# Optimization experiments

Measured on AMD Instinct MI355X. Metric: run time of the kernel, lower is better.

Reference implementation:

```python
import jax, jax.numpy as jnp
import numpy as np

EPS = 1e-12  # torch F.normalize eps

def _l2norm(v, axis):
    n = jnp.sqrt(jnp.sum(v * v, axis=axis, keepdims=True))
    return v / jnp.maximum(n, EPS)

def setup_inputs() -> dict:
    key = jax.random.key(0)
    k1, k2, k3 = jax.random.split(key, 3)
    B, D, H, W, K = 64, 512, 30, 40, 64
    x = jax.random.normal(k1, (B, D, H, W), dtype=jnp.float32)
    conv_w = jax.random.normal(k2, (K, D), dtype=jnp.float32)  # 1x1 conv weight, no bias (vladv1)
    centroids = jax.random.uniform(k3, (K, D), dtype=jnp.float32)
    return {"x": x, "conv_w": conv_w, "centroids": centroids}

def reference(x, conv_w, centroids):
    B, D, H, W = x.shape
    K = centroids.shape[0]
    # L2-normalize input descriptors over channel dim
    x = _l2norm(x, axis=1)
    xf = x.reshape(B, D, H * W)                       # (B, D, N)
    # 1x1 conv == per-pixel matmul; softmax over clusters
    logits = jnp.einsum('bdn,kd->bkn', xf, conv_w)    # (B, K, N)
    a = jax.nn.softmax(logits, axis=1)                # (B, K, N)
    # VLAD residual aggregation, loop-free:
    # vlad[b,k,d] = sum_n a[b,k,n] * (x[b,d,n] - c[k,d])
    vlad = jnp.einsum('bkn,bdn->bkd', a, xf) - a.sum(axis=-1)[..., None] * centroids[None]
    # intra-normalize per cluster, flatten, global L2 norm
    vlad = _l2norm(vlad, axis=2)
    v = vlad.reshape(B, K * D)
    return _l2norm(v, axis=1)
```

## Files before the change

### kernel.cpp

```cpp
#include <hip/hip_runtime.h>

#define B_ 64
#define D_ 512
#define N_ 1200
#define K_ 64
#define NT2CNT 19
#define AST 1216
#define NT3 16
#define PT 32
#define NTILES 38

typedef unsigned short u16;
typedef __attribute__((ext_vector_type(8))) short bf16x8;
typedef __attribute__((ext_vector_type(8))) unsigned short u16x8;
typedef __attribute__((ext_vector_type(4))) float f32x4;

__device__ __forceinline__ float bf2f(u16 u) {
  union { unsigned int i; float f; } v; v.i = ((unsigned int)u) << 16; return v.f;
}
__device__ __forceinline__ u16 f2bf(float f) {
  unsigned int u = __float_as_uint(f);
  u += 0x7FFFu + ((u >> 16) & 1u);
  return (u16)(u >> 16);
}

__global__ __launch_bounds__(64) void k_wsplit(
    const float* __restrict__ w,
    u16* __restrict__ wfh, u16* __restrict__ wfl)
{
  const int blk = blockIdx.x;
  const int wv = blk >> 4, kk = blk & 15;
  const int l = threadIdx.x;
  const int row = wv * 16 + (l & 15);
  const int dbase = kk * 32 + 8 * (l >> 4);
  const size_t o = ((size_t)blk * 64 + l) * 8;
#pragma unroll
  for (int j = 0; j < 8; ++j) {
    const float v = w[row * D_ + dbase + j];
    const unsigned int u = __float_as_uint(v);
    const unsigned int h = u & 0xFFFF0000u;
    wfh[o + j] = (u16)(h >> 16);
    wfl[o + j] = f2bf(v - __uint_as_float(h));
  }
}

__global__ __launch_bounds__(256, 4) void k_logits_mfma(
    const float* __restrict__ x, const u16* __restrict__ wfh,
    const u16* __restrict__ wfl, u16* __restrict__ a_bf,
    float* __restrict__ invn_ws, float* __restrict__ asum_part, int folded)
{
  const int nt = blockIdx.x, b = blockIdx.y;
  const int n0 = nt * 64;
  const int t = threadIdx.x;
  const int lane = t & 63, wv = t >> 6;

  __shared__ __align__(16) u16 xbuf[2][2][512][8];
  __shared__ float nsq_s[4][64];
  __shared__ float red_s[3][64];
  float (*ls)[66] = reinterpret_cast<float(*)[66]>(&xbuf[0][0][0][0]);

  const int n_l = t & 63, dg = t >> 6;
  const int nc = min(n0 + n_l, N_ - 1);
  const float* xb = x + (size_t)b * D_ * N_ + nc;
  float nsq = 0.f;

  f32x4 acc[4] = {{0.f,0.f,0.f,0.f},{0.f,0.f,0.f,0.f},{0.f,0.f,0.f,0.f},{0.f,0.f,0.f,0.f}};

  const int kkl_w = dg >> 1;
  const int qb    = (dg & 1) * 2;
  const int slotw = kkl_w * 256 + (n_l >> 4) * 64 + qb * 16 + (n_l & 15);

  auto loadf = [&](int c, float* f) {
    const int db = c * 64 + dg * 16;
#pragma unroll
    for (int e = 0; e < 16; ++e) f[e] = xb[(size_t)(db + e) * N_];
  };
  auto cvtwrite = [&](const float* f, int buf) {
    u16x8 h0{}, h1{}, l0{}, l1{};
#pragma unroll
    for (int e = 0; e < 16; ++e) {
      nsq += f[e] * f[e];
      const unsigned int u = __float_as_uint(f[e]);
      const unsigned int hi = u & 0xFFFF0000u;
      const u16 hh = (u16)(hi >> 16);
      const u16 ll = f2bf(f[e] - __uint_as_float(hi));
      if (e < 8) { h0[e] = (short)hh; l0[e] = (short)ll; }
      else       { h1[e - 8] = (short)hh; l1[e - 8] = (short)ll; }
    }
    *(u16x8*)xbuf[buf][0][slotw]      = h0;
    *(u16x8*)xbuf[buf][0][slotw + 16] = h1;
    *(u16x8*)xbuf[buf][1][slotw]      = l0;
    *(u16x8*)xbuf[buf][1][slotw + 16] = l1;
  };
  auto mstep = [&](int c, int buf) {
#pragma unroll
    for (int kkl = 0; kkl < 2; ++kkl) {
      const int fi = (wv * 16 + c * 2 + kkl) * 64 + lane;
      const bf16x8 ah = ((const bf16x8*)wfh)[fi];
      const bf16x8 al = ((const bf16x8*)wfl)[fi];
#pragma unroll
      for (int s = 0; s < 4; ++s) {
        const bf16x8 bh = *(const bf16x8*)xbuf[buf][0][kkl * 256 + s * 64 + lane];
        const bf16x8 bl = *(const bf16x8*)xbuf[buf][1][kkl * 256 + s * 64 + lane];
        acc[s] = __builtin_amdgcn_mfma_f32_16x16x32_bf16(ah, bh, acc[s], 0, 0, 0);
        acc[s] = __builtin_amdgcn_mfma_f32_16x16x32_bf16(al, bh, acc[s], 0, 0, 0);
        acc[s] = __builtin_amdgcn_mfma_f32_16x16x32_bf16(ah, bl, acc[s], 0, 0, 0);
      }
    }
  };

  { float f[16]; loadf(0, f); cvtwrite(f, 0); }
  __syncthreads();
#pragma unroll
  for (int c = 0; c < 8; ++c) {
    float f[16];
    if (c < 7) loadf(c + 1, f);
    mstep(c, c & 1);
    if (c < 7) cvtwrite(f, (c + 1) & 1);
    __syncthreads();
  }

  nsq_s[dg][n_l] = nsq;
  __syncthreads();
  if (t < 64) {
    const float s4 = nsq_s[0][t] + nsq_s[1][t] + nsq_s[2][t] + nsq_s[3][t];
    const float inv = 1.f / fmaxf(sqrtf(s4), 1e-12f);
    red_s[0][t] = inv;
    if (n0 + t < N_) invn_ws[b * N_ + t + n0] = inv;
  }
  __syncthreads();

#pragma unroll
  for (int s = 0; s < 4; ++s) {
    const int n = 16 * s + (lane & 15);
    const float inv = red_s[0][n];
#pragma unroll
    for (int r = 0; r < 4; ++r) {
      const int k = 16 * wv + 4 * (lane >> 4) + r;
      ls[k][n] = acc[s][r] * inv;
    }
  }
  __syncthreads();

  if (t < 64) {
    float m = -1e30f;
    for (int k = 0; k < K_; ++k) m = fmaxf(m, ls[k][t]);
    float ssum = 0.f;
    for (int k = 0; k < K_; ++k) ssum += __expf(ls[k][t] - m);
    red_s[1][t] = m;
    red_s[2][t] = 1.f / ssum;
  }
  __syncthreads();

#pragma unroll
  for (int s = 0; s < 4; ++s) {
    const int n = 16 * s + (lane & 15);
    const bool valid = (n0 + n) < N_;
    const float inv = red_s[0][n], mv = red_s[1][n], si = red_s[2][n];
#pragma unroll
    for (int r = 0; r < 4; ++r) {
      const int k = 16 * wv + 4 * (lane >> 4) + r;
      const float av = valid ? __expf(acc[s][r] * inv - mv) * si : 0.f;
      ls[k][n] = av;
      if (folded) {
        a_bf[((size_t)b * K_ + k) * AST + n0 + n] = f2bf(av * inv);
      } else if (valid) {
        a_bf[((size_t)b * K_ + k) * N_ + n0 + n] = f2bf(av);
      }
    }
  }
  __syncthreads();

  if (t < K_) {
    float su = 0.f;
#pragma unroll 8
    for (int p = 0; p < 64; ++p) su += ls[t][p];
    asum_part[(b * NT2CNT + nt) * K_ + t] = su;
  }
}

__global__ __launch_bounds__(256, 4) void k_vlad_mfma(
    const float* __restrict__ x, const u16* __restrict__ a_bf,
    float* __restrict__ vlad_ws)
{
  const int id = blockIdx.x;
  const int b  = id >> 3;
  const int dc = (id >> 1) & 3;
  const int ns = id & 1;
  const int t = threadIdx.x;
  const int lane = t & 63, wv = t >> 6;

  __shared__ __align__(16) u16 xs[2][2][512][8];

  f32x4 acc[8];
#pragma unroll
  for (int i = 0; i < 8; ++i) acc[i] = (f32x4){0.f, 0.f, 0.f, 0.f};

  const int sr = t >> 1, sh = t & 1;
  const float* xrow = x + (size_t)b * D_ * N_ + (size_t)(dc * 128 + sr) * N_;
  const int slotw = (sr >> 4) * 64 + (sh * 2) * 16 + (sr & 15);

  auto loadf = [&](int s, float4* vr) {
    const int nb = (ns * 19 + s) * 32 + sh * 16;
#pragma unroll
    for (int i = 0; i < 4; ++i) {
      const int nn = nb + 4 * i;
      vr[i] = (nn < N_) ? *(const float4*)(xrow + nn)
                        : make_float4(0.f, 0.f, 0.f, 0.f);
    }
  };
  auto cvtwrite = [&](const float4* vr, int buf) {
    u16x8 h0{}, h1{}, l0{}, l1{};
#pragma unroll
    for (int i = 0; i < 4; ++i) {
      const float fv[4] = {vr[i].x, vr[i].y, vr[i].z, vr[i].w};
#pragma unroll
      for (int j = 0; j < 4; ++j) {
        const int e = 4 * i + j;
        const unsigned int u = __float_as_uint(fv[j]);
        const unsigned int hi = u & 0xFFFF0000u;
        const u16 hh = (u16)(hi >> 16);
        const u16 ll = f2bf(fv[j] - __uint_as_float(hi));
        if (e < 8) { h0[e] = (short)hh; l0[e] = (short)ll; }
        else       { h1[e - 8] = (short)hh; l1[e - 8] = (short)ll; }
      }
    }
    *(u16x8*)xs[buf][0][slotw]      = h0;
    *(u16x8*)xs[buf][0][slotw + 16] = h1;
    *(u16x8*)xs[buf][1][slotw]      = l0;
    *(u16x8*)xs[buf][1][slotw + 16] = l1;
  };

  const u16* arow = a_bf + ((size_t)b * K_ + 16 * wv + (lane & 15)) * AST + 8 * (lane >> 4);

  auto compute = [&](int s, int buf) {
    const bf16x8 af = *(const bf16x8*)(arow + (ns * 19 + s) * 32);
#pragma unroll
    for (int st = 0; st < 8; ++st) {
      const bf16x8 bh = *(const bf16x8*)xs[buf][0][st * 64 + lane];
      const bf16x8 bl = *(const bf16x8*)xs[buf][1][st * 64 + lane];
      acc[st] = __builtin_amdgcn_mfma_f32_16x16x32_bf16(af, bh, acc[st], 0, 0, 0);
      acc[st] = __builtin_amdgcn_mfma_f32_16x16x32_bf16(af, bl, acc[st], 0, 0, 0);
    }
  };

  { float4 vr[4]; loadf(0, vr); cvtwrite(vr, 0); }
  __syncthreads();
#pragma unroll 2
  for (int s = 0; s < 19; ++s) {
    float4 vr[4];
    if (s < 18) loadf(s + 1, vr);
    compute(s, s & 1);
    if (s < 18) cvtwrite(vr, (s + 1) & 1);
    __syncthreads();
  }

  float* vp = vlad_ws + (size_t)ns * B_ * K_ * D_;
  const size_t kb = (size_t)b * K_ + 16 * wv + 4 * (lane >> 4);
  const int db = dc * 128 + (lane & 15);
#pragma unroll
  for (int st = 0; st < 8; ++st)
#pragma unroll
    for (int r = 0; r < 4; ++r)
      vp[(kb + r) * D_ + db + st * 16] = acc[st][r];
}

__global__ __launch_bounds__(256) void k_norm(
    const float* __restrict__ vlad_ws, const float* __restrict__ asum_part,
    const float* __restrict__ cent, float* __restrict__ out)
{
  const int id = blockIdx.x;
  const int kg = id >> 6;
  const int b  = id & 63;
  const int t  = threadIdx.x;
  __shared__ float asums[8];
  __shared__ float part[8][4];
  __shared__ float scale_s[8];

  if (t < 8) {
    float s = 0.f;
    for (int nt2 = 0; nt2 < NT2CNT; ++nt2)
      s += asum_part[(b * NT2CNT + nt2) * K_ + kg * 8 + t];
    asums[t] = s;
  }
  __syncthreads();

  const int d0 = 2 * t;
  const int lane = t & 63, wv = t >> 6;
  const size_t vhalf = (size_t)B_ * K_ * D_;
  float acc[16];
#pragma unroll
  for (int j = 0; j < 8; ++j) {
    const int k = kg * 8 + j;
    const size_t vofs = ((size_t)b * K_ + k) * D_ + d0;
    const float2 v0 = *(const float2*)(vlad_ws + vofs);
    const float2 v1 = *(const float2*)(vlad_ws + vhalf + vofs);
    const float2 c2 = *(const float2*)(cent + (size_t)k * D_ + d0);
    const float asv = asums[j];
    acc[j * 2]     = v0.x + v1.x - asv * c2.x;
    acc[j * 2 + 1] = v0.y + v1.y - asv * c2.y;
    float s = acc[j * 2] * acc[j * 2] + acc[j * 2 + 1] * acc[j * 2 + 1];
#pragma unroll
    for (int o = 32; o > 0; o >>= 1) s += __shfl_down(s, o, 64);
    if (lane == 0) part[j][wv] = s;
  }
  __syncthreads();
  if (t < 8) {
    const float s = part[t][0] + part[t][1] + part[t][2] + part[t][3];
    scale_s[t] = 0.125f / fmaxf(sqrtf(s), 1e-12f);
  }
  __syncthreads();
#pragma unroll
  for (int j = 0; j < 8; ++j) {
    const int k = kg * 8 + j;
    const float f = scale_s[j];
    float2 o;
    o.x = acc[j * 2] * f;
    o.y = acc[j * 2 + 1] * f;
    *(float2*)(out + ((size_t)b * K_ + k) * D_ + d0) = o;
  }
}

__global__ __launch_bounds__(256) void k_vlad(
    const float* __restrict__ x, const u16* __restrict__ a_bf,
    const float* __restrict__ invn_ws, const float* __restrict__ asum_part,
    const float* __restrict__ cent, float* __restrict__ out)
{
  const int id = blockIdx.x;
  const int kg = id >> 6;
  const int b  = id & 63;
  const int t  = threadIdx.x;
  __shared__ float xs[NT3][518];
  __shared__ float as[8][NT3 + 2];
  __shared__ float asums[8];
  __shared__ float part[8][4];
  __shared__ float scale_s[8];

  if (t < 8) {
    float s = 0.f;
    for (int nt2 = 0; nt2 < NT2CNT; ++nt2)
      s += asum_part[(b * NT2CNT + nt2) * K_ + kg * 8 + t];
    asums[t] = s;
  }
  float acc[16];
#pragma unroll
  for (int i = 0; i < 16; ++i) acc[i] = 0.f;

  const float* xb = x + (size_t)b * D_ * N_;
  const int d0 = 2 * t;
  const int snl = t & 15, sdc = t >> 4;
  const int saj = t >> 4, sanl = t & 15;

  for (int n0 = 0; n0 < N_; n0 += NT3) {
    __syncthreads();
    {
      const float* xp = xb + (size_t)(sdc * 32) * N_ + (n0 + snl);
      float* xrow = &xs[snl][sdc * 32];
#pragma unroll
      for (int i = 0; i < 32; i += 2) {
        float2 w2;
        w2.x = xp[(size_t)i * N_];
        w2.y = xp[(size_t)(i + 1) * N_];
        *(float2*)(xrow + i) = w2;
      }
    }
    if (t < 128) {
      const float av = bf2f(a_bf[((size_t)b * K_ + kg * 8 + saj) * N_ + n0 + sanl])
                     * invn_ws[b * N_ + n0 + sanl];
      as[saj][sanl] = av;
    }
    __syncthreads();
#pragma unroll 2
    for (int nl = 0; nl < NT3; nl += 2) {
      const float2 x0 = *(const float2*)(&xs[nl][d0]);
      const float2 x1 = *(const float2*)(&xs[nl + 1][d0]);
#pragma unroll
      for (int j = 0; j < 8; ++j) {
        const float2 a2 = *(const float2*)(&as[j][nl]);
        acc[j * 2]     = fmaf(a2.x, x0.x, fmaf(a2.y, x1.x, acc[j * 2]));
        acc[j * 2 + 1] = fmaf(a2.x, x0.y, fmaf(a2.y, x1.y, acc[j * 2 + 1]));
      }
    }
  }
  __syncthreads();
  const int lane = t & 63, wv = t >> 6;
#pragma unroll
  for (int j = 0; j < 8; ++j) {
    const int k = kg * 8 + j;
    const float asv = asums[j];
    const float2 c2 = *(const float2*)(cent + (size_t)k * D_ + d0);
    acc[j * 2]     -= asv * c2.x;
    acc[j * 2 + 1] -= asv * c2.y;
    float v = acc[j * 2] * acc[j * 2] + acc[j * 2 + 1] * acc[j * 2 + 1];
#pragma unroll
    for (int o = 32; o > 0; o >>= 1) v += __shfl_down(v, o, 64);
    if (lane == 0) part[j][wv] = v;
  }
  __syncthreads();
  if (t < 8) {
    const float s = part[t][0] + part[t][1] + part[t][2] + part[t][3];
    scale_s[t] = 0.125f / fmaxf(sqrtf(s), 1e-12f);
  }
  __syncthreads();
#pragma unroll
  for (int j = 0; j < 8; ++j) {
    const int k = kg * 8 + j;
    const float f = scale_s[j];
    float2 o;
    o.x = acc[j * 2] * f;
    o.y = acc[j * 2 + 1] * f;
    *(float2*)(out + ((size_t)b * K_ + k) * D_ + d0) = o;
  }
}

__global__ __launch_bounds__(256) void k_logits(
    const float* __restrict__ x, const float* __restrict__ w,
    u16* __restrict__ a_bf, float* __restrict__ invn_ws,
    float* __restrict__ asum_part)
{
  const int nt = blockIdx.x, b = blockIdx.y;
  const int t = threadIdx.x;
  const int px = t & 63;
  const int kg = t >> 6;
  const int n = nt * 64 + px;
  const bool valid = (n < N_);
  const int nc = valid ? n : (N_ - 1);
  __shared__ float lsh[K_][65];

  const float* xb = x + (size_t)b * D_ * N_ + nc;
  const float* wg = w + kg * 16 * D_;

  float acc[16];
#pragma unroll
  for (int j = 0; j < 16; ++j) acc[j] = 0.f;
  float nsq = 0.f;

  for (int d = 0; d < D_; d += 4) {
    const float xv0 = xb[(size_t)(d + 0) * N_];
    const float xv1 = xb[(size_t)(d + 1) * N_];
    const float xv2 = xb[(size_t)(d + 2) * N_];
    const float xv3 = xb[(size_t)(d + 3) * N_];
    nsq += xv0 * xv0 + xv1 * xv1 + xv2 * xv2 + xv3 * xv3;
#pragma unroll
    for (int j = 0; j < 16; ++j) {
      const float4 wv = *(const float4*)(wg + j * D_ + d);
      acc[j] = fmaf(xv0, wv.x, fmaf(xv1, wv.y, fmaf(xv2, wv.z, fmaf(xv3, wv.w, acc[j]))));
    }
  }
  const float invn = 1.f / fmaxf(sqrtf(nsq), 1e-12f);
  if (kg == 0 && valid) invn_ws[b * N_ + n] = invn;
#pragma unroll
  for (int j = 0; j < 16; ++j) lsh[kg * 16 + j][px] = acc[j] * invn;
  __syncthreads();
  float m = -1e30f;
  for (int k = 0; k < K_; ++k) m = fmaxf(m, lsh[k][px]);
  float s = 0.f;
  for (int k = 0; k < K_; ++k) s += __expf(lsh[k][px] - m);
  const float sinv = 1.f / s;
  float av[16];
#pragma unroll
  for (int j = 0; j < 16; ++j)
    av[j] = valid ? __expf(acc[j] * invn - m) * sinv : 0.f;
  __syncthreads();
#pragma unroll
  for (int j = 0; j < 16; ++j) lsh[kg * 16 + j][px] = av[j];
  if (valid) {
#pragma unroll
    for (int j = 0; j < 16; ++j)
      a_bf[((size_t)b * K_ + kg * 16 + j) * N_ + n] = f2bf(av[j]);
  }
  __syncthreads();
  if (t < K_) {
    float su = 0.f;
#pragma unroll 8
    for (int p = 0; p < 64; ++p) su += lsh[t][p];
    asum_part[(b * NT2CNT + nt) * K_ + t] = su;
  }
}

__global__ __launch_bounds__(256) void k_fused(
    const float* __restrict__ x, const float* __restrict__ w,
    const float* __restrict__ cent, float* __restrict__ out)
{
  const int id = blockIdx.x;
  const int kq = id >> 6;
  const int b  = id & 63;
  const int t  = threadIdx.x;
  const int px = t & 31;
  const int kg = t >> 5;
  const bool own = (kg >> 1) == kq;
  const int khbase = (kg & 1) * 8;

  __shared__ u16 xs[PT][514];
  __shared__ float ls[K_][33];
  __shared__ float a_s[16][34];
  __shared__ float araw[16][34];
  __shared__ float asums[16];
  __shared__ float part[16][4];
  __shared__ float scale_s[16];

  if (t < 16) asums[t] = 0.f;
  float acc[32];
#pragma unroll
  for (int i = 0; i < 32; ++i) acc[i] = 0.f;
  const float* xb = x + (size_t)b * D_ * N_;

  for (int tile = 0; tile < NTILES; ++tile) {
    const int n0 = tile * PT;
    {
      const int row = t & 31, chunk = t >> 5;
      const int n = n0 + row;
      const int nc = (n < N_) ? n : (N_ - 1);
      const float* xp = xb + (size_t)(chunk * 64) * N_ + nc;
#pragma unroll
      for (int i = 0; i < 64; ++i)
        xs[row][chunk * 64 + i] = f2bf(xp[(size_t)i * N_]);
    }
    __syncthreads();
    float invn;
    {
      const ushort2* xr = (const ushort2*)xs[px];
      float lg[8] = {0,0,0,0,0,0,0,0};
      float nsq = 0.f;
      const float* wbase = w + (size_t)(kg * 8) * D_;
      for (int du = 0; du < D_ / 4; ++du) {
        const ushort2 p0 = xr[2 * du], p1 = xr[2 * du + 1];
        const float x0 = bf2f(p0.x), x1 = bf2f(p0.y), x2 = bf2f(p1.x), x3 = bf2f(p1.y);
        nsq += x0 * x0 + x1 * x1 + x2 * x2 + x3 * x3;
#pragma unroll
        for (int j = 0; j < 8; ++j) {
          const float4 wv = *(const float4*)(wbase + j * D_ + 4 * du);
          lg[j] = fmaf(x0,wv.x,fmaf(x1,wv.y,fmaf(x2,wv.z,fmaf(x3,wv.w,lg[j]))));
        }
      }
      invn = 1.f / fmaxf(sqrtf(nsq), 1e-12f);
#pragma unroll
      for (int j = 0; j < 8; ++j) ls[kg * 8 + j][px] = lg[j] * invn;
    }
    __syncthreads();
    {
      const bool valid = (n0 + px) < N_;
      float m = -1e30f;
      for (int k = 0; k < K_; ++k) m = fmaxf(m, ls[k][px]);
      float s = 0.f;
      for (int k = 0; k < K_; ++k) s += __expf(ls[k][px] - m);
      const float sinv = 1.f / s;
      if (own) {
#pragma unroll
        for (int j = 0; j < 8; ++j) {
          const float av = valid ? __expf(ls[kg * 8 + j][px] - m) * sinv : 0.f;
          araw[khbase + j][px] = av;
          a_s[khbase + j][px]  = av * invn;
        }
      }
    }
    __syncthreads();
    if (t < 16) {
      float su = 0.f;
#pragma unroll 8
      for (int p = 0; p < PT; ++p) su += araw[t][p];
      asums[t] += su;
    }
    {
#pragma unroll 2
      for (int nl = 0; nl < PT; nl += 2) {
        const ushort2 u0 = ((const ushort2*)xs[nl])[t];
        const ushort2 u1 = ((const ushort2*)xs[nl + 1])[t];
        const float x00 = bf2f(u0.x), x01 = bf2f(u0.y);
        const float x10 = bf2f(u1.x), x11 = bf2f(u1.y);
#pragma unroll
        for (int kh = 0; kh < 16; ++kh) {
          const float2 a2 = *(const float2*)(&a_s[kh][nl]);
          acc[kh * 2]     = fmaf(a2.x, x00, fmaf(a2.y, x10, acc[kh * 2]));
          acc[kh * 2 + 1] = fmaf(a2.x, x01, fmaf(a2.y, x11, acc[kh * 2 + 1]));
        }
      }
    }
    __syncthreads();
  }
  const int d0 = 2 * t;
  const int lane = t & 63, wv = t >> 6;
#pragma unroll
  for (int kh = 0; kh < 16; ++kh) {
    const int k = kq * 16 + kh;
    const float asv = asums[kh];
    const float2 c2 = *(const float2*)(cent + (size_t)k * D_ + d0);
    acc[kh * 2]     -= asv * c2.x;
    acc[kh * 2 + 1] -= asv * c2.y;
    float v = acc[kh * 2] * acc[kh * 2] + acc[kh * 2 + 1] * acc[kh * 2 + 1];
#pragma unroll
    for (int o = 32; o > 0; o >>= 1) v += __shfl_down(v, o, 64);
    if (lane == 0) part[kh][wv] = v;
  }
  __syncthreads();
  if (t < 16) {
    const float s = part[t][0] + part[t][1] + part[t][2] + part[t][3];
    scale_s[t] = 0.125f / fmaxf(sqrtf(s), 1e-12f);
  }
  __syncthreads();
#pragma unroll
  for (int kh = 0; kh < 16; ++kh) {
    const int k = kq * 16 + kh;
    const float f = scale_s[kh];
    float2 o;
    o.x = acc[kh * 2] * f;
    o.y = acc[kh * 2 + 1] * f;
    *(float2*)(out + ((size_t)b * K_ + k) * D_ + d0) = o;
  }
}

extern "C" void kernel_launch(void* const* d_in, const int* in_sizes, int n_in,
                              void* d_out, int out_size, void* d_ws, size_t ws_size,
                              hipStream_t stream)
{
  const float* x  = (const float*)d_in[0];
  const float* w  = (const float*)d_in[1];
  const float* ct = (const float*)d_in[2];
  float* out = (float*)d_out;

  const size_t wf_u16  = (size_t)K_ * D_;
  const size_t invn_f  = (size_t)B_ * N_;
  const size_t asum_f  = (size_t)B_ * NT2CNT * K_;
  const size_t a_u16   = (size_t)B_ * K_ * N_;
  const size_t ap_u16  = (size_t)B_ * K_ * AST;
  const size_t vlad_f  = (size_t)B_ * K_ * D_;
  const size_t need_old  = (invn_f + asum_f) * 4 + a_u16 * 2;
  const size_t need_mfma = need_old + wf_u16 * 2 * 2;
  const size_t need_v2   = wf_u16 * 2 * 2 + ap_u16 * 2
                         + (invn_f + asum_f + vlad_f * 2) * 4;

  if (ws_size >= need_v2) {
    u16* wfh = (u16*)d_ws;
    u16* wfl = wfh + wf_u16;
    u16* a_bf = wfl + wf_u16;
    float* invn_ws   = (float*)(a_bf + ap_u16);
    float* asum_part = invn_ws + invn_f;
    float* vlad_ws   = asum_part + asum_f;
    hipLaunchKernelGGL(k_wsplit, dim3(64), dim3(64), 0, stream, w, wfh, wfl);
    hipLaunchKernelGGL(k_logits_mfma, dim3(NT2CNT, B_), dim3(256), 0, stream,
                       x, wfh, wfl, a_bf, invn_ws, asum_part, 1);
    hipLaunchKernelGGL(k_vlad_mfma, dim3(512), dim3(256), 0, stream,
                       x, a_bf, vlad_ws);
    hipLaunchKernelGGL(k_norm, dim3(512), dim3(256), 0, stream,
                       vlad_ws, asum_part, ct, out);
  } else if (ws_size >= need_mfma) {
    u16* wfh = (u16*)d_ws;
    u16* wfl = wfh + wf_u16;
    float* invn_ws   = (float*)(wfl + wf_u16);
    float* asum_part = invn_ws + invn_f;
    u16* a_bf = (u16*)(asum_part + asum_f);
    hipLaunchKernelGGL(k_wsplit, dim3(64), dim3(64), 0, stream, w, wfh, wfl);
    hipLaunchKernelGGL(k_logits_mfma, dim3(NT2CNT, B_), dim3(256), 0, stream,
                       x, wfh, wfl, a_bf, invn_ws, asum_part, 0);
    hipLaunchKernelGGL(k_vlad, dim3(512), dim3(256), 0, stream,
                       x, a_bf, invn_ws, asum_part, ct, out);
  } else if (ws_size >= need_old) {
    float* invn_ws   = (float*)d_ws;
    float* asum_part = invn_ws + invn_f;
    u16* a_bf = (u16*)(asum_part + asum_f);
    hipLaunchKernelGGL(k_logits, dim3(NT2CNT, B_), dim3(256), 0, stream,
                       x, w, a_bf, invn_ws, asum_part);
    hipLaunchKernelGGL(k_vlad, dim3(512), dim3(256), 0, stream,
                       x, a_bf, invn_ws, asum_part, ct, out);
  } else {
    hipLaunchKernelGGL(k_fused, dim3(256), dim3(256), 0, stream, x, w, ct, out);
  }
}
```

Measured before the change: 287.2 us.

## Split VLAD N-reduction four ways and prefetch MFMA operand fragments

The VLAD MFMA kernel now splits the pixel dimension into four chunks instead of two, doubling the grid to 1024 blocks. The norm kernel sums four partial results instead of two. Both MFMA kernels also prefetch weight or assignment fragments one or two steps ahead of their use, and the bf16 hi/lo split is repacked per half-vector. The goal is more parallelism on the GPU and less load latency exposed in the MFMA loops. The cost is twice the partial-sum workspace traffic, plus a workspace requirement large enough that it could push execution onto a fallback path.

```diff
diff --git a/kernel.cpp b/kernel.cpp
--- a/kernel.cpp
+++ b/kernel.cpp
@@ -76,46 +76,54 @@
     for (int e = 0; e < 16; ++e) f[e] = xb[(size_t)(db + e) * N_];
   };
   auto cvtwrite = [&](const float* f, int buf) {
-    u16x8 h0{}, h1{}, l0{}, l1{};
-#pragma unroll
-    for (int e = 0; e < 16; ++e) {
-      nsq += f[e] * f[e];
-      const unsigned int u = __float_as_uint(f[e]);
-      const unsigned int hi = u & 0xFFFF0000u;
-      const u16 hh = (u16)(hi >> 16);
-      const u16 ll = f2bf(f[e] - __uint_as_float(hi));
-      if (e < 8) { h0[e] = (short)hh; l0[e] = (short)ll; }
-      else       { h1[e - 8] = (short)hh; l1[e - 8] = (short)ll; }
-    }
-    *(u16x8*)xbuf[buf][0][slotw]      = h0;
-    *(u16x8*)xbuf[buf][0][slotw + 16] = h1;
-    *(u16x8*)xbuf[buf][1][slotw]      = l0;
-    *(u16x8*)xbuf[buf][1][slotw + 16] = l1;
-  };
-  auto mstep = [&](int c, int buf) {
+#pragma unroll
+    for (int half = 0; half < 2; ++half) {
+      u16x8 hv{}, lv{};
+#pragma unroll
+      for (int e = 0; e < 8; ++e) {
+        const float fe = f[half * 8 + e];
+        nsq += fe * fe;
+        const unsigned int u = __float_as_uint(fe);
+        const unsigned int hi = u & 0xFFFF0000u;
+        hv[e] = (short)(u16)(hi >> 16);
+        lv[e] = (short)f2bf(fe - __uint_as_float(hi));
+      }
+      *(u16x8*)xbuf[buf][0][slotw + half * 16] = hv;
+      *(u16x8*)xbuf[buf][1][slotw + half * 16] = lv;
+    }
+  };
+  auto loadw = [&](int c, bf16x8 (&wf)[2][2]) {
 #pragma unroll
     for (int kkl = 0; kkl < 2; ++kkl) {
       const int fi = (wv * 16 + c * 2 + kkl) * 64 + lane;
-      const bf16x8 ah = ((const bf16x8*)wfh)[fi];
-      const bf16x8 al = ((const bf16x8*)wfl)[fi];
+      wf[kkl][0] = ((const bf16x8*)wfh)[fi];
+      wf[kkl][1] = ((const bf16x8*)wfl)[fi];
+    }
+  };
+  auto mstep = [&](int buf, const bf16x8 (&wf)[2][2]) {
+#pragma unroll
+    for (int kkl = 0; kkl < 2; ++kkl)
 #pragma unroll
       for (int s = 0; s < 4; ++s) {
         const bf16x8 bh = *(const bf16x8*)xbuf[buf][0][kkl * 256 + s * 64 + lane];
         const bf16x8 bl = *(const bf16x8*)xbuf[buf][1][kkl * 256 + s * 64 + lane];
-        acc[s] = __builtin_amdgcn_mfma_f32_16x16x32_bf16(ah, bh, acc[s], 0, 0, 0);
-        acc[s] = __builtin_amdgcn_mfma_f32_16x16x32_bf16(al, bh, acc[s], 0, 0, 0);
-        acc[s] = __builtin_amdgcn_mfma_f32_16x16x32_bf16(ah, bl, acc[s], 0, 0, 0);
-      }
-    }
-  };
-
+        acc[s] = __builtin_amdgcn_mfma_f32_16x16x32_bf16(wf[kkl][0], bh, acc[s], 0, 0, 0);
+        acc[s] = __builtin_amdgcn_mfma_f32_16x16x32_bf16(wf[kkl][1], bh, acc[s], 0, 0, 0);
+        acc[s] = __builtin_amdgcn_mfma_f32_16x16x32_bf16(wf[kkl][0], bl, acc[s], 0, 0, 0);
+      }
+  };
+
+  bf16x8 wfrag[2][2][2];
+  loadw(0, wfrag[0]);
+  loadw(1, wfrag[1]);
   { float f[16]; loadf(0, f); cvtwrite(f, 0); }
   __syncthreads();
 #pragma unroll
   for (int c = 0; c < 8; ++c) {
     float f[16];
     if (c < 7) loadf(c + 1, f);
-    mstep(c, c & 1);
+    mstep(c & 1, wfrag[c & 1]);
+    if (c < 6) loadw(c + 2, wfrag[c & 1]);
     if (c < 7) cvtwrite(f, (c + 1) & 1);
     __syncthreads();
   }
@@ -184,9 +192,13 @@
     float* __restrict__ vlad_ws)
 {
   const int id = blockIdx.x;
-  const int b  = id >> 3;
-  const int dc = (id >> 1) & 3;
-  const int ns = id & 1;
+  const int b  = id >> 4;
+  const int dc = (id >> 2) & 3;
+  const int ns = id & 3;
+  const int s0 = ns * 10;
+  const int s1 = (ns == 3) ? 38 : s0 + 10;
+  const int sl = s1 - 1;
+  const int m  = s1 - s0;
   const int t = threadIdx.x;
   const int lane = t & 63, wv = t >> 6;
 
@@ -201,7 +213,7 @@
   const int slotw = (sr >> 4) * 64 + (sh * 2) * 16 + (sr & 15);
 
   auto loadf = [&](int s, float4* vr) {
-    const int nb = (ns * 19 + s) * 32 + sh * 16;
+    const int nb = s * 32 + sh * 16;
 #pragma unroll
     for (int i = 0; i < 4; ++i) {
       const int nn = nb + 4 * i;
@@ -210,31 +222,30 @@
     }
   };
   auto cvtwrite = [&](const float4* vr, int buf) {
-    u16x8 h0{}, h1{}, l0{}, l1{};
-#pragma unroll
-    for (int i = 0; i < 4; ++i) {
-      const float fv[4] = {vr[i].x, vr[i].y, vr[i].z, vr[i].w};
-#pragma unroll
-      for (int j = 0; j < 4; ++j) {
-        const int e = 4 * i + j;
-        const unsigned int u = __float_as_uint(fv[j]);
-        const unsigned int hi = u & 0xFFFF0000u;
-        const u16 hh = (u16)(hi >> 16);
-        const u16 ll = f2bf(fv[j] - __uint_as_float(hi));
-        if (e < 8) { h0[e] = (short)hh; l0[e] = (short)ll; }
-        else       { h1[e - 8] = (short)hh; l1[e - 8] = (short)ll; }
-      }
-    }
-    *(u16x8*)xs[buf][0][slotw]      = h0;
-    *(u16x8*)xs[buf][0][slotw + 16] = h1;
-    *(u16x8*)xs[buf][1][slotw]      = l0;
-    *(u16x8*)xs[buf][1][slotw + 16] = l1;
+#pragma unroll
+    for (int half = 0; half < 2; ++half) {
+      u16x8 hv{}, lv{};
+#pragma unroll
+      for (int i = 0; i < 2; ++i) {
+        const float4 v = vr[half * 2 + i];
+        const float fv[4] = {v.x, v.y, v.z, v.w};
+#pragma unroll
+        for (int j = 0; j < 4; ++j) {
+          const unsigned int u = __float_as_uint(fv[j]);
+          const unsigned int hi = u & 0xFFFF0000u;
+          hv[i * 4 + j] = (short)(u16)(hi >> 16);
+          lv[i * 4 + j] = (short)f2bf(fv[j] - __uint_as_float(hi));
+        }
+      }
+      *(u16x8*)xs[buf][0][slotw + half * 16] = hv;
+      *(u16x8*)xs[buf][1][slotw + half * 16] = lv;
+    }
   };
 
   const u16* arow = a_bf + ((size_t)b * K_ + 16 * wv + (lane & 15)) * AST + 8 * (lane >> 4);
-
-  auto compute = [&](int s, int buf) {
-    const bf16x8 af = *(const bf16x8*)(arow + (ns * 19 + s) * 32);
+  auto loadA = [&](int s) -> bf16x8 { return *(const bf16x8*)(arow + s * 32); };
+
+  auto compute = [&](const bf16x8& af, int buf) {
 #pragma unroll
     for (int st = 0; st < 8; ++st) {
       const bf16x8 bh = *(const bf16x8*)xs[buf][0][st * 64 + lane];
@@ -244,15 +255,22 @@
     }
   };
 
-  { float4 vr[4]; loadf(0, vr); cvtwrite(vr, 0); }
-  __syncthreads();
-#pragma unroll 2
-  for (int s = 0; s < 19; ++s) {
+  auto body = [&](int s, bf16x8& af, int br) {
     float4 vr[4];
-    if (s < 18) loadf(s + 1, vr);
-    compute(s, s & 1);
-    if (s < 18) cvtwrite(vr, (s + 1) & 1);
-    __syncthreads();
+    loadf(min(s + 1, sl), vr);
+    compute(af, br);
+    af = loadA(min(s + 2, sl));
+    cvtwrite(vr, br ^ 1);
+    __syncthreads();
+  };
+
+  bf16x8 afA = loadA(s0);
+  bf16x8 afB = loadA(min(s0 + 1, sl));
+  { float4 vr[4]; loadf(s0, vr); cvtwrite(vr, 0); }
+  __syncthreads();
+  for (int j = 0; j < m; j += 2) {
+    body(s0 + j, afA, 0);
+    body(s0 + j + 1, afB, 1);
   }
 
   float* vp = vlad_ws + (size_t)ns * B_ * K_ * D_;
@@ -287,18 +305,22 @@
 
   const int d0 = 2 * t;
   const int lane = t & 63, wv = t >> 6;
-  const size_t vhalf = (size_t)B_ * K_ * D_;
+  const size_t vstride = (size_t)B_ * K_ * D_;
   float acc[16];
 #pragma unroll
   for (int j = 0; j < 8; ++j) {
     const int k = kg * 8 + j;
     const size_t vofs = ((size_t)b * K_ + k) * D_ + d0;
-    const float2 v0 = *(const float2*)(vlad_ws + vofs);
-    const float2 v1 = *(const float2*)(vlad_ws + vhalf + vofs);
+    float2 vs = {0.f, 0.f};
+#pragma unroll
+    for (int p = 0; p < 4; ++p) {
+      const float2 v = *(const float2*)(vlad_ws + p * vstride + vofs);
+      vs.x += v.x; vs.y += v.y;
+    }
     const float2 c2 = *(const float2*)(cent + (size_t)k * D_ + d0);
     const float asv = asums[j];
-    acc[j * 2]     = v0.x + v1.x - asv * c2.x;
-    acc[j * 2 + 1] = v0.y + v1.y - asv * c2.y;
+    acc[j * 2]     = vs.x - asv * c2.x;
+    acc[j * 2 + 1] = vs.y - asv * c2.y;
     float s = acc[j * 2] * acc[j * 2] + acc[j * 2 + 1] * acc[j * 2 + 1];
 #pragma unroll
     for (int o = 32; o > 0; o >>= 1) s += __shfl_down(s, o, 64);
@@ -627,7 +649,7 @@
   const size_t need_old  = (invn_f + asum_f) * 4 + a_u16 * 2;
   const size_t need_mfma = need_old + wf_u16 * 2 * 2;
   const size_t need_v2   = wf_u16 * 2 * 2 + ap_u16 * 2
-                         + (invn_f + asum_f + vlad_f * 2) * 4;
+                         + (invn_f + asum_f + vlad_f * 4) * 4;
 
   if (ws_size >= need_v2) {
     u16* wfh = (u16*)d_ws;
@@ -639,7 +661,7 @@
     hipLaunchKernelGGL(k_wsplit, dim3(64), dim3(64), 0, stream, w, wfh, wfl);
     hipLaunchKernelGGL(k_logits_mfma, dim3(NT2CNT, B_), dim3(256), 0, stream,
                        x, wfh, wfl, a_bf, invn_ws, asum_part, 1);
-    hipLaunchKernelGGL(k_vlad_mfma, dim3(512), dim3(256), 0, stream,
+    hipLaunchKernelGGL(k_vlad_mfma, dim3(1024), dim3(256), 0, stream,
                        x, a_bf, vlad_ws);
     hipLaunchKernelGGL(k_norm, dim3(512), dim3(256), 0, stream,
                        vlad_ws, asum_part, ct, out);
```

After: 286.6 us. Within noise of the previous version (-0.2%).
